# Kernel tuning notes

Hardware: AMD Instinct MI355X
Metric: run time of the kernel (lower is better)

The kernel has to match this reference:

```python
import jax, jax.numpy as jnp
import numpy as np

DEPTH = 11          # tree depth
D = 1024            # input_width
H = 32              # hidden_width (leaf MLP)
O = 1024            # output_width
B = 4096            # flattened token batch
N_LEAVES = 2 ** DEPTH
N_NODES = 2 ** DEPTH - 1


def setup_inputs() -> dict:
    key = jax.random.key(0)
    ks = jax.random.split(key, 7)
    f1 = 1.0 / np.sqrt(D)
    f2 = 1.0 / np.sqrt(H)
    u = lambda k, shape, f: jax.random.uniform(k, shape, jnp.float32, -f, f)
    return {
        "x": jax.random.normal(ks[0], (B, D), jnp.float32),
        "node_weights": u(ks[1], (N_NODES, D), f1),
        "node_biases": u(ks[2], (N_NODES,), f1),   # (n_nodes,1) in torch; flattened
        "w1s": u(ks[3], (N_LEAVES, D, H), f1),
        "b1s": u(ks[4], (N_LEAVES, H), f1),
        "w2s": u(ks[5], (N_LEAVES, H, O), f2),
        "b2s": u(ks[6], (N_LEAVES, O), f2),
    }


def reference(x, node_weights, node_biases, w1s, b1s, w2s, b2s):
    # --- hard tree descent (eval_forward) ---
    nodes = jnp.zeros((x.shape[0],), jnp.int32)
    for i in range(DEPTH):  # fixed small loop over tree depth
        w = node_weights[nodes]                       # [B, D] gathered plane coeffs
        b = node_biases[nodes]                        # [B]
        score = jnp.einsum('bd,bd->b', x, w) + b      # per-sample dot product
        choice = (score >= 0).astype(jnp.int32)
        platform = 2 ** i - 1
        next_platform = 2 ** (i + 1) - 1
        nodes = (nodes - platform) * 2 + choice + next_platform
    leaves = nodes - (2 ** DEPTH - 1)                 # [B] leaf index per sample

    # --- per-sample leaf MLP with gathered weights ---
    h = jax.nn.relu(jnp.einsum('bd,bdh->bh', x, w1s[leaves]) + b1s[leaves])  # [B, H]
    out = jnp.einsum('bh,bho->bo', h, w2s[leaves]) + b2s[leaves]             # [B, O]
    return out
```

## Files before the change

kernel.cpp:

```cpp
#include <hip/hip_runtime.h>

#define DEPTH 11
#define D 1024
#define H 32
#define OW 1024
#define B 4096
#define N_LEAVES 2048
#define N_NODES 2047
#define SMAX 4
#define MAX_ITEMS 3072
#define CHUNKF 4096

typedef __attribute__((address_space(3))) void lds_void;
typedef const __attribute__((address_space(1))) void glb_void;

__global__ __launch_bounds__(256) void descent_kernel(
    const float* __restrict__ x, const float* __restrict__ nw,
    const float* __restrict__ nb, int* __restrict__ leaf,
    int* __restrict__ rnk, int* __restrict__ count)
{
    int lane = threadIdx.x & 63;
    int wv   = threadIdx.x >> 6;
    int samp = blockIdx.x * 4 + wv;

    const float4* xp = (const float4*)(x + (size_t)samp * D);
    float4 xf[4];
#pragma unroll
    for (int k = 0; k < 4; k++) xf[k] = xp[lane + 64 * k];

    int node = 0;
#pragma unroll
    for (int i = 0; i < DEPTH; i++) {
        const float4* wp = (const float4*)(nw + (size_t)node * D);
        double s = 0.0;
#pragma unroll
        for (int k = 0; k < 4; k++) {
            float4 wf = wp[lane + 64 * k];
            s += (double)xf[k].x * (double)wf.x;
            s += (double)xf[k].y * (double)wf.y;
            s += (double)xf[k].z * (double)wf.z;
            s += (double)xf[k].w * (double)wf.w;
        }
#pragma unroll
        for (int m = 32; m >= 1; m >>= 1) s += __shfl_xor(s, m, 64);
        double score = s + (double)nb[node];
        int choice = (score >= 0.0) ? 1 : 0;
        node = 2 * node + 1 + choice;
    }
    int lf = node - N_NODES;
    if (lane == 0) {
        leaf[samp] = lf;
        rnk[samp]  = atomicAdd(&count[lf], 1);
    }
}

__global__ __launch_bounds__(256) void scan_kernel(
    const int* __restrict__ count, int* __restrict__ offsets)
{
    __shared__ int tot[256];
    int t = threadIdx.x;
    int c[8], s = 0;
#pragma unroll
    for (int k = 0; k < 8; k++) { c[k] = count[t * 8 + k]; s += c[k]; }
    tot[t] = s;
    __syncthreads();
    for (int off = 1; off < 256; off <<= 1) {
        int v = (t >= off) ? tot[t - off] : 0;
        __syncthreads();
        tot[t] += v;
        __syncthreads();
    }
    int base = (t > 0) ? tot[t - 1] : 0;
#pragma unroll
    for (int k = 0; k < 8; k++) { offsets[t * 8 + k] = base; base += c[k]; }
}

__global__ __launch_bounds__(256) void scatter_kernel(
    const int* __restrict__ leaf, const int* __restrict__ rnk,
    const int* __restrict__ offsets, int* __restrict__ bucket)
{
    int i = blockIdx.x * 256 + threadIdx.x;
    bucket[offsets[leaf[i]] + rnk[i]] = i;
}

__global__ __launch_bounds__(256) void build_items_kernel(
    const int* __restrict__ count, int* __restrict__ items,
    int* __restrict__ nitems)
{
    int l = blockIdx.x * 256 + threadIdx.x;
    int c = count[l];
    if (c > 0) {
        int k = (c + SMAX - 1) / SMAX;
        int base = atomicAdd(nitems, k);
        for (int i = 0; i < k; i++)
            items[base + i] = l | ((i * SMAX) << 11);
    }
}

__device__ __forceinline__ void stage16k(const float* __restrict__ src,
                                         float* ldsbase, int wave, int lane)
{
#pragma unroll
    for (int i = 0; i < 4; i++) {
        const float* g = src + wave * 1024 + i * 256 + lane * 4;
        float*       l = ldsbase + wave * 1024 + i * 256;
        __builtin_amdgcn_global_load_lds((glb_void*)g, (lds_void*)l, 16, 0, 0);
    }
}

template <int SS>
__device__ __forceinline__ void mlp_item(
    int tid, const float* __restrict__ x, const float* __restrict__ w1,
    const float* __restrict__ w2, const float* __restrict__ b1,
    const float* __restrict__ b2, const int* __restrict__ bucket, int base,
    float (*xs)[D], float* wbuf, float (*pl1)[32][SMAX], float (*hs)[H],
    float* __restrict__ out)
{
    const int lane = tid & 63, wave = tid >> 6;
    const int jq = tid & 7, dg = tid >> 3;

    int sid[SS];
#pragma unroll
    for (int s = 0; s < SS; s++) sid[s] = bucket[base + s];

#pragma unroll
    for (int s = 0; s < SS; s++) {
        const float* g = x + (size_t)sid[s] * D + wave * 256 + lane * 4;
        float*       l = xs[s] + wave * 256;
        __builtin_amdgcn_global_load_lds((glb_void*)g, (lds_void*)l, 16, 0, 0);
    }
    stage16k(w1, wbuf, wave, lane);
    __syncthreads();

    float4 acc[SS];
#pragma unroll
    for (int s = 0; s < SS; s++) acc[s] = make_float4(0.f, 0.f, 0.f, 0.f);

    for (int c = 0; c < 8; c++) {
        const float* nsrc = (c < 7) ? (w1 + (c + 1) * CHUNKF) : w2;
        stage16k(nsrc, wbuf + ((c + 1) & 1) * CHUNKF, wave, lane);
        const float* wb = wbuf + (c & 1) * CHUNKF;
        int d0 = c * 128;
#pragma unroll
        for (int k = 0; k < 4; k++) {
            int r = dg + (k << 5);
            float4 w = *(const float4*)(wb + r * 32 + jq * 4);
#pragma unroll
            for (int s = 0; s < SS; s++) {
                float xv = xs[s][d0 + r];
                acc[s].x += xv * w.x;
                acc[s].y += xv * w.y;
                acc[s].z += xv * w.z;
                acc[s].w += xv * w.w;
            }
        }
        __syncthreads();
    }

#pragma unroll
    for (int m = 8; m <= 32; m <<= 1)
#pragma unroll
        for (int s = 0; s < SS; s++) {
            acc[s].x += __shfl_xor(acc[s].x, m, 64);
            acc[s].y += __shfl_xor(acc[s].y, m, 64);
            acc[s].z += __shfl_xor(acc[s].z, m, 64);
            acc[s].w += __shfl_xor(acc[s].w, m, 64);
        }
    if (lane < 8) {
#pragma unroll
        for (int s = 0; s < SS; s++) {
            pl1[wave][jq * 4 + 0][s] = acc[s].x;
            pl1[wave][jq * 4 + 1][s] = acc[s].y;
            pl1[wave][jq * 4 + 2][s] = acc[s].z;
            pl1[wave][jq * 4 + 3][s] = acc[s].w;
        }
    }
    __syncthreads();
    if (tid < 32 * SS) {
        int s2 = tid >> 5, j2 = tid & 31;
        float sum = pl1[0][j2][s2] + pl1[1][j2][s2] + pl1[2][j2][s2] +
                    pl1[3][j2][s2] + b1[j2];
        hs[s2][j2] = fmaxf(sum, 0.f);
    }
    __syncthreads();

    float4 o[SS];
#pragma unroll
    for (int s = 0; s < SS; s++) o[s] = make_float4(0.f, 0.f, 0.f, 0.f);

    for (int c = 0; c < 8; c++) {
        if (c < 7)
            stage16k(w2 + (c + 1) * CHUNKF, wbuf + ((c + 1) & 1) * CHUNKF, wave, lane);
        const float* wb = wbuf + (c & 1) * CHUNKF;
        int j0 = c * 4;
#pragma unroll
        for (int jj = 0; jj < 4; jj++) {
            float4 w = *(const float4*)(wb + jj * 1024 + tid * 4);
#pragma unroll
            for (int s = 0; s < SS; s++) {
                float hv = hs[s][j0 + jj];
                o[s].x += hv * w.x;
                o[s].y += hv * w.y;
                o[s].z += hv * w.z;
                o[s].w += hv * w.w;
            }
        }
        __syncthreads();
    }

    float4 bv = ((const float4*)b2)[tid];
#pragma unroll
    for (int s = 0; s < SS; s++) {
        float4 o4;
        o4.x = o[s].x + bv.x;
        o4.y = o[s].y + bv.y;
        o4.z = o[s].z + bv.z;
        o4.w = o[s].w + bv.w;
        ((float4*)(out + (size_t)sid[s] * OW))[tid] = o4;
    }
}

__global__ __launch_bounds__(256) void mlp_kernel(
    const float* __restrict__ x, const float* __restrict__ w1s,
    const float* __restrict__ b1s, const float* __restrict__ w2s,
    const float* __restrict__ b2s, const int* __restrict__ offsets,
    const int* __restrict__ count, const int* __restrict__ bucket,
    const int* __restrict__ items, const int* __restrict__ nitems,
    float* __restrict__ out)
{
    __shared__ float xs[SMAX][D];
    __shared__ float wbuf[2][CHUNKF];
    __shared__ float pl1[4][32][SMAX];
    __shared__ float hs[SMAX][H];

    if ((int)blockIdx.x >= nitems[0]) return;
    int item  = items[blockIdx.x];
    int l     = item & (N_LEAVES - 1);
    int start = item >> 11;
    int S     = min(SMAX, count[l] - start);
    int base  = offsets[l] + start;
    int tid   = threadIdx.x;

    const float* w1 = w1s + (size_t)l * D * H;
    const float* w2 = w2s + (size_t)l * H * OW;
    const float* b1 = b1s + (size_t)l * H;
    const float* b2 = b2s + (size_t)l * OW;

    switch (S) {
        case 1: mlp_item<1>(tid, x, w1, w2, b1, b2, bucket, base, xs, &wbuf[0][0], pl1, hs, out); break;
        case 2: mlp_item<2>(tid, x, w1, w2, b1, b2, bucket, base, xs, &wbuf[0][0], pl1, hs, out); break;
        case 3: mlp_item<3>(tid, x, w1, w2, b1, b2, bucket, base, xs, &wbuf[0][0], pl1, hs, out); break;
        default: mlp_item<4>(tid, x, w1, w2, b1, b2, bucket, base, xs, &wbuf[0][0], pl1, hs, out); break;
    }
}

extern "C" void kernel_launch(void* const* d_in, const int* in_sizes, int n_in,
                              void* d_out, int out_size, void* d_ws, size_t ws_size,
                              hipStream_t stream)
{
    const float* x   = (const float*)d_in[0];
    const float* nw  = (const float*)d_in[1];
    const float* nb  = (const float*)d_in[2];
    const float* w1s = (const float*)d_in[3];
    const float* b1s = (const float*)d_in[4];
    const float* w2s = (const float*)d_in[5];
    const float* b2s = (const float*)d_in[6];
    float* out = (float*)d_out;

    int* leaf    = (int*)d_ws;
    int* rnk     = leaf + B;
    int* count   = rnk + B;
    int* offsets = count + N_LEAVES;
    int* bucket  = offsets + N_LEAVES;
    int* items   = bucket + B;
    int* nitems  = items + MAX_ITEMS;

    hipMemsetAsync(count, 0, N_LEAVES * sizeof(int), stream);
    hipMemsetAsync(nitems, 0, sizeof(int), stream);
    descent_kernel<<<B / 4, 256, 0, stream>>>(x, nw, nb, leaf, rnk, count);
    scan_kernel<<<1, 256, 0, stream>>>(count, offsets);
    scatter_kernel<<<B / 256, 256, 0, stream>>>(leaf, rnk, offsets, bucket);
    build_items_kernel<<<N_LEAVES / 256, 256, 0, stream>>>(count, items, nitems);
    mlp_kernel<<<MAX_ITEMS, 256, 0, stream>>>(x, w1s, b1s, w2s, b2s,
                                              offsets, count, bucket,
                                              items, nitems, out);
}
```

Before: 131.8 us.

## Give each wave private triple-buffered weight staging with vmcnt waits instead of block barriers

Each wave now streams its own slice of the leaf weights (W1 by D-range, W2 by output columns) through a private three-slot LDS ring. Hand-placed s_waitcnt vmcnt fences replace the per-chunk __syncthreads, so waves no longer stall on one another and more loads stay in flight. W2 prefetch now starts before the layer-1 cross-wave reduction, the bias load is hoisted, and launch bounds ask for 2 blocks per CU. The cost is more LDS (48 KB of weight buffers) and correctness that depends on exact counts of outstanding loads.

```diff
diff --git a/kernel.cpp b/kernel.cpp
--- a/kernel.cpp
+++ b/kernel.cpp
@@ -9,10 +9,14 @@
 #define N_NODES 2047
 #define SMAX 4
 #define MAX_ITEMS 3072
-#define CHUNKF 4096
 
 typedef __attribute__((address_space(3))) void lds_void;
 typedef const __attribute__((address_space(1))) void glb_void;
+
+#define WAITV8  do { asm volatile("s_waitcnt vmcnt(8)" ::: "memory"); __builtin_amdgcn_sched_barrier(0); } while (0)
+#define WAITV4  do { asm volatile("s_waitcnt vmcnt(4)" ::: "memory"); __builtin_amdgcn_sched_barrier(0); } while (0)
+#define WAITV0  do { asm volatile("s_waitcnt vmcnt(0)" ::: "memory"); __builtin_amdgcn_sched_barrier(0); } while (0)
+#define WAITLG0 do { asm volatile("s_waitcnt lgkmcnt(0)" ::: "memory"); __builtin_amdgcn_sched_barrier(0); } while (0)
 
 __global__ __launch_bounds__(256) void descent_kernel(
     const float* __restrict__ x, const float* __restrict__ nw,
@@ -97,14 +101,56 @@
     }
 }
 
-__device__ __forceinline__ void stage16k(const float* __restrict__ src,
-                                         float* ldsbase, int wave, int lane)
-{
-#pragma unroll
-    for (int i = 0; i < 4; i++) {
-        const float* g = src + wave * 1024 + i * 256 + lane * 4;
-        float*       l = ldsbase + wave * 1024 + i * 256;
-        __builtin_amdgcn_global_load_lds((glb_void*)g, (lds_void*)l, 16, 0, 0);
+__device__ __forceinline__ void stage4k(const float* src, float* dst, int lane)
+{
+#pragma unroll
+    for (int i = 0; i < 4; i++)
+        __builtin_amdgcn_global_load_lds((glb_void*)(src + i * 256 + lane * 4),
+                                         (lds_void*)(dst + i * 256), 16, 0, 0);
+}
+
+__device__ __forceinline__ void stageL2(const float* w2w, int cj, float* dst, int lane)
+{
+#pragma unroll
+    for (int jl = 0; jl < 4; jl++)
+        __builtin_amdgcn_global_load_lds(
+            (glb_void*)(w2w + (size_t)(cj * 4 + jl) * OW + lane * 4),
+            (lds_void*)(dst + jl * 256), 16, 0, 0);
+}
+
+template <int SS>
+__device__ __forceinline__ void l1c(const float* p, const float* xsw, int c,
+                                    int lane, int dg, float4* acc)
+{
+#pragma unroll
+    for (int u = 0; u < 4; u++) {
+        float4 w = ((const float4*)p)[u * 64 + lane];
+#pragma unroll
+        for (int s = 0; s < SS; s++) {
+            float xv = xsw[s * D + c * 32 + u * 8 + dg];
+            acc[s].x += xv * w.x;
+            acc[s].y += xv * w.y;
+            acc[s].z += xv * w.z;
+            acc[s].w += xv * w.w;
+        }
+    }
+}
+
+template <int SS>
+__device__ __forceinline__ void l2c(const float* p, const float (*hs)[H], int cj,
+                                    int lane, float4* o)
+{
+#pragma unroll
+    for (int jl = 0; jl < 4; jl++) {
+        float4 w = ((const float4*)p)[jl * 64 + lane];
+#pragma unroll
+        for (int s = 0; s < SS; s++) {
+            float hv = hs[s][cj * 4 + jl];
+            o[s].x += hv * w.x;
+            o[s].y += hv * w.y;
+            o[s].z += hv * w.z;
+            o[s].w += hv * w.w;
+        }
     }
 }
 
@@ -113,49 +159,43 @@
     int tid, const float* __restrict__ x, const float* __restrict__ w1,
     const float* __restrict__ w2, const float* __restrict__ b1,
     const float* __restrict__ b2, const int* __restrict__ bucket, int base,
-    float (*xs)[D], float* wbuf, float (*pl1)[32][SMAX], float (*hs)[H],
+    float* xs, float* wq, float (*pl1)[SMAX][32], float (*hs)[H],
     float* __restrict__ out)
 {
     const int lane = tid & 63, wave = tid >> 6;
-    const int jq = tid & 7, dg = tid >> 3;
+    const int jq = lane & 7, dg = lane >> 3;
+
+    float b1v = b1[tid & 31];
+    asm volatile("" :: "v"(b1v));
 
     int sid[SS];
 #pragma unroll
     for (int s = 0; s < SS; s++) sid[s] = bucket[base + s];
 
 #pragma unroll
-    for (int s = 0; s < SS; s++) {
-        const float* g = x + (size_t)sid[s] * D + wave * 256 + lane * 4;
-        float*       l = xs[s] + wave * 256;
-        __builtin_amdgcn_global_load_lds((glb_void*)g, (lds_void*)l, 16, 0, 0);
-    }
-    stage16k(w1, wbuf, wave, lane);
-    __syncthreads();
+    for (int s = 0; s < SS; s++)
+        __builtin_amdgcn_global_load_lds(
+            (glb_void*)(x + (size_t)sid[s] * D + wave * 256 + lane * 4),
+            (lds_void*)(xs + s * D + wave * 256), 16, 0, 0);
+
+    const float* w1w = w1 + wave * 8192;
+    const float* xsw = xs + wave * 256;
+    stage4k(w1w + 0 * 1024, wq + 0 * 1024, lane);
+    stage4k(w1w + 1 * 1024, wq + 1 * 1024, lane);
+    stage4k(w1w + 2 * 1024, wq + 2 * 1024, lane);
 
     float4 acc[SS];
 #pragma unroll
     for (int s = 0; s < SS; s++) acc[s] = make_float4(0.f, 0.f, 0.f, 0.f);
 
-    for (int c = 0; c < 8; c++) {
-        const float* nsrc = (c < 7) ? (w1 + (c + 1) * CHUNKF) : w2;
-        stage16k(nsrc, wbuf + ((c + 1) & 1) * CHUNKF, wave, lane);
-        const float* wb = wbuf + (c & 1) * CHUNKF;
-        int d0 = c * 128;
-#pragma unroll
-        for (int k = 0; k < 4; k++) {
-            int r = dg + (k << 5);
-            float4 w = *(const float4*)(wb + r * 32 + jq * 4);
-#pragma unroll
-            for (int s = 0; s < SS; s++) {
-                float xv = xs[s][d0 + r];
-                acc[s].x += xv * w.x;
-                acc[s].y += xv * w.y;
-                acc[s].z += xv * w.z;
-                acc[s].w += xv * w.w;
-            }
-        }
-        __syncthreads();
-    }
+    WAITV8; l1c<SS>(wq + 0 * 1024, xsw, 0, lane, dg, acc); stage4k(w1w + 3 * 1024, wq + 0 * 1024, lane);
+    WAITV8; l1c<SS>(wq + 1 * 1024, xsw, 1, lane, dg, acc); stage4k(w1w + 4 * 1024, wq + 1 * 1024, lane);
+    WAITV8; l1c<SS>(wq + 2 * 1024, xsw, 2, lane, dg, acc); stage4k(w1w + 5 * 1024, wq + 2 * 1024, lane);
+    WAITV8; l1c<SS>(wq + 0 * 1024, xsw, 3, lane, dg, acc); stage4k(w1w + 6 * 1024, wq + 0 * 1024, lane);
+    WAITV8; l1c<SS>(wq + 1 * 1024, xsw, 4, lane, dg, acc); stage4k(w1w + 7 * 1024, wq + 1 * 1024, lane);
+    WAITV8; l1c<SS>(wq + 2 * 1024, xsw, 5, lane, dg, acc);
+    WAITV4; l1c<SS>(wq + 0 * 1024, xsw, 6, lane, dg, acc);
+    WAITV0; l1c<SS>(wq + 1 * 1024, xsw, 7, lane, dg, acc);
 
 #pragma unroll
     for (int m = 8; m <= 32; m <<= 1)
@@ -166,49 +206,42 @@
             acc[s].z += __shfl_xor(acc[s].z, m, 64);
             acc[s].w += __shfl_xor(acc[s].w, m, 64);
         }
-    if (lane < 8) {
-#pragma unroll
-        for (int s = 0; s < SS; s++) {
-            pl1[wave][jq * 4 + 0][s] = acc[s].x;
-            pl1[wave][jq * 4 + 1][s] = acc[s].y;
-            pl1[wave][jq * 4 + 2][s] = acc[s].z;
-            pl1[wave][jq * 4 + 3][s] = acc[s].w;
-        }
-    }
-    __syncthreads();
+    if (dg == 0) {
+#pragma unroll
+        for (int s = 0; s < SS; s++)
+            *(float4*)&pl1[wave][s][jq * 4] = acc[s];
+    }
+
+    const float* w2w = w2 + wave * 256;
+    stageL2(w2w, 0, wq + 0 * 1024, lane);
+    stageL2(w2w, 1, wq + 1 * 1024, lane);
+    stageL2(w2w, 2, wq + 2 * 1024, lane);
+
+    WAITLG0;
+    __builtin_amdgcn_s_barrier();
     if (tid < 32 * SS) {
         int s2 = tid >> 5, j2 = tid & 31;
-        float sum = pl1[0][j2][s2] + pl1[1][j2][s2] + pl1[2][j2][s2] +
-                    pl1[3][j2][s2] + b1[j2];
+        float sum = pl1[0][s2][j2] + pl1[1][s2][j2] + pl1[2][s2][j2] +
+                    pl1[3][s2][j2] + b1v;
         hs[s2][j2] = fmaxf(sum, 0.f);
     }
-    __syncthreads();
+    WAITLG0;
+    __builtin_amdgcn_s_barrier();
 
     float4 o[SS];
 #pragma unroll
     for (int s = 0; s < SS; s++) o[s] = make_float4(0.f, 0.f, 0.f, 0.f);
 
-    for (int c = 0; c < 8; c++) {
-        if (c < 7)
-            stage16k(w2 + (c + 1) * CHUNKF, wbuf + ((c + 1) & 1) * CHUNKF, wave, lane);
-        const float* wb = wbuf + (c & 1) * CHUNKF;
-        int j0 = c * 4;
-#pragma unroll
-        for (int jj = 0; jj < 4; jj++) {
-            float4 w = *(const float4*)(wb + jj * 1024 + tid * 4);
-#pragma unroll
-            for (int s = 0; s < SS; s++) {
-                float hv = hs[s][j0 + jj];
-                o[s].x += hv * w.x;
-                o[s].y += hv * w.y;
-                o[s].z += hv * w.z;
-                o[s].w += hv * w.w;
-            }
-        }
-        __syncthreads();
-    }
-
-    float4 bv = ((const float4*)b2)[tid];
+    WAITV8; l2c<SS>(wq + 0 * 1024, hs, 0, lane, o); stageL2(w2w, 3, wq + 0 * 1024, lane);
+    WAITV8; l2c<SS>(wq + 1 * 1024, hs, 1, lane, o); stageL2(w2w, 4, wq + 1 * 1024, lane);
+    WAITV8; l2c<SS>(wq + 2 * 1024, hs, 2, lane, o); stageL2(w2w, 5, wq + 2 * 1024, lane);
+    WAITV8; l2c<SS>(wq + 0 * 1024, hs, 3, lane, o); stageL2(w2w, 6, wq + 0 * 1024, lane);
+    WAITV8; l2c<SS>(wq + 1 * 1024, hs, 4, lane, o); stageL2(w2w, 7, wq + 1 * 1024, lane);
+    WAITV8; l2c<SS>(wq + 2 * 1024, hs, 5, lane, o);
+    WAITV4; l2c<SS>(wq + 0 * 1024, hs, 6, lane, o);
+    WAITV0; l2c<SS>(wq + 1 * 1024, hs, 7, lane, o);
+
+    float4 bv = *(const float4*)(b2 + wave * 256 + lane * 4);
 #pragma unroll
     for (int s = 0; s < SS; s++) {
         float4 o4;
@@ -216,11 +249,11 @@
         o4.y = o[s].y + bv.y;
         o4.z = o[s].z + bv.z;
         o4.w = o[s].w + bv.w;
-        ((float4*)(out + (size_t)sid[s] * OW))[tid] = o4;
-    }
-}
-
-__global__ __launch_bounds__(256) void mlp_kernel(
+        *(float4*)(out + (size_t)sid[s] * OW + wave * 256 + lane * 4) = o4;
+    }
+}
+
+__global__ __launch_bounds__(256, 2) void mlp_kernel(
     const float* __restrict__ x, const float* __restrict__ w1s,
     const float* __restrict__ b1s, const float* __restrict__ w2s,
     const float* __restrict__ b2s, const int* __restrict__ offsets,
@@ -228,9 +261,9 @@
     const int* __restrict__ items, const int* __restrict__ nitems,
     float* __restrict__ out)
 {
-    __shared__ float xs[SMAX][D];
-    __shared__ float wbuf[2][CHUNKF];
-    __shared__ float pl1[4][32][SMAX];
+    __shared__ float xs[SMAX * D];
+    __shared__ float wbuf[4 * 3 * 1024];
+    __shared__ float pl1[4][SMAX][32];
     __shared__ float hs[SMAX][H];
 
     if ((int)blockIdx.x >= nitems[0]) return;
@@ -245,12 +278,13 @@
     const float* w2 = w2s + (size_t)l * H * OW;
     const float* b1 = b1s + (size_t)l * H;
     const float* b2 = b2s + (size_t)l * OW;
+    float* wq = wbuf + (tid >> 6) * 3 * 1024;
 
     switch (S) {
-        case 1: mlp_item<1>(tid, x, w1, w2, b1, b2, bucket, base, xs, &wbuf[0][0], pl1, hs, out); break;
-        case 2: mlp_item<2>(tid, x, w1, w2, b1, b2, bucket, base, xs, &wbuf[0][0], pl1, hs, out); break;
-        case 3: mlp_item<3>(tid, x, w1, w2, b1, b2, bucket, base, xs, &wbuf[0][0], pl1, hs, out); break;
-        default: mlp_item<4>(tid, x, w1, w2, b1, b2, bucket, base, xs, &wbuf[0][0], pl1, hs, out); break;
+        case 1: mlp_item<1>(tid, x, w1, w2, b1, b2, bucket, base, xs, wq, pl1, hs, out); break;
+        case 2: mlp_item<2>(tid, x, w1, w2, b1, b2, bucket, base, xs, wq, pl1, hs, out); break;
+        case 3: mlp_item<3>(tid, x, w1, w2, b1, b2, bucket, base, xs, wq, pl1, hs, out); break;
+        default: mlp_item<4>(tid, x, w1, w2, b1, b2, bucket, base, xs, wq, pl1, hs, out); break;
     }
 }
 
```

After: 125.9 us. 4.5% less time.
